# Optimization experiments

Measured on AMD Instinct MI355X. Metric: run time of the kernel, lower is better.

Reference implementation:

```python
import jax, jax.numpy as jnp
import numpy as np

T, N, K, E = 5, 2048, 20, 512
H, AI, BL, G1, G2, U = 64, 32, 64, 64, 64, 8
SLOPE, ALPHA = 0.01, 1.0


def gru(x, Wih, Whh, bih, bhh):
    # batch_first torch nn.GRU with h0 = 0. x: [B, L, I] -> [B, L, Hd]
    Hd = Whh.shape[1]
    def step(h, xt):
        gi = xt @ Wih.T + bih
        gh = h @ Whh.T + bhh
        ir, iz, in_ = jnp.split(gi, 3, axis=-1)
        hr, hz, hn = jnp.split(gh, 3, axis=-1)
        r = jax.nn.sigmoid(ir + hr)
        z = jax.nn.sigmoid(iz + hz)
        n = jnp.tanh(in_ + r * hn)
        h_new = (1.0 - z) * n + z * h
        return h_new, h_new
    h0 = jnp.zeros((x.shape[0], Hd), x.dtype)
    _, ys = jax.lax.scan(step, h0, jnp.swapaxes(x, 0, 1))
    return jnp.swapaxes(ys, 0, 1)


def lin_attn(x, w1, b1, w2):
    # LinearAttention: softmax over dim=2 (weights_size=1), then bmm -> [B,1,H]
    inter = jnp.tanh(x @ w1.T + b1)
    w = jax.nn.softmax(inter @ w2.T, axis=2)  # [B,L,1]
    return jnp.einsum('blk,blh->bkh', w, x)


def sgat_multi(x, W, a, adj):
    # All U SGAT heads at once. Decompose a^T [Wh_i || Wh_j] = s1_i + s2_j
    # (same math as the dense NxNx2F construction, without materializing it).
    O = W.shape[-1]
    Wh = jnp.einsum('nf,ufo->uno', x, W)                 # [U,N,O]
    s1 = jnp.einsum('uno,uo->un', Wh, a[:, :O, 0])
    s2 = jnp.einsum('uno,uo->un', Wh, a[:, O:, 0])
    e = jax.nn.leaky_relu(s1[:, :, None] + s2[:, None, :], SLOPE)  # [U,N,N]
    e = jnp.where(adj[None, :, :] > 0, e, -9e15)
    att = jax.nn.softmax(e, axis=2)
    h = jnp.einsum('unm,umo->uno', att, Wh)              # [U,N,O]
    # torch.cat over heads along feature dim -> [N, U*O]
    return jnp.transpose(h, (1, 0, 2)).reshape(x.shape[0], -1)


def setup_inputs() -> dict:
    key = jax.random.key(0)
    ks = iter(jax.random.split(key, 40))
    def nrm(shape, scale=0.1):
        return jax.random.normal(next(ks), shape, dtype=jnp.float32) * scale
    d = {}
    d['p'] = nrm((N, T, 3), 1.0)
    d['m'] = nrm((T, N, K, E), 1.0)
    adj = (jax.random.uniform(next(ks), (N, N)) < 0.05).astype(jnp.float32)
    d['adj'] = jnp.maximum(adj, jnp.eye(N, dtype=jnp.float32))
    d['Wih_p'] = nrm((3 * H, 3)); d['Whh_p'] = nrm((3 * H, H))
    d['bih_p'] = nrm((3 * H,)); d['bhh_p'] = nrm((3 * H,))
    d['Wih_m'] = nrm((3 * H, E)); d['Whh_m'] = nrm((3 * H, H))
    d['bih_m'] = nrm((3 * H,)); d['bhh_m'] = nrm((3 * H,))
    d['Wih_s'] = nrm((3 * H, H)); d['Whh_s'] = nrm((3 * H, H))
    d['bih_s'] = nrm((3 * H,)); d['bhh_s'] = nrm((3 * H,))
    for pref in ('ap', 'am', 'as'):
        d[pref + '_w1'] = nrm((AI, H)); d[pref + '_b1'] = nrm((AI,))
        d[pref + '_w2'] = nrm((1, AI))
    d['blend_W'] = nrm((BL, H, H)); d['blend_b'] = nrm((BL,))
    d['g1_W'] = nrm((U, BL, G1)); d['g1_a'] = nrm((U, 2 * G1, 1))
    d['g2_W'] = nrm((U, U * G1, G2)); d['g2_a'] = nrm((U, 2 * G2, 1))
    d['fin_W'] = nrm((1, U * G2)); d['fin_b'] = nrm((1,))
    return d


def reference(p, m, adj, Wih_p, Whh_p, bih_p, bhh_p, Wih_m, Whh_m, bih_m, bhh_m,
              Wih_s, Whh_s, bih_s, bhh_s, ap_w1, ap_b1, ap_w2, am_w1, am_b1, am_w2,
              as_w1, as_b1, as_w2, blend_W, blend_b, g1_W, g1_a, g2_W, g2_a,
              fin_W, fin_b):
    h_p = gru(p, Wih_p, Whh_p, bih_p, bhh_p)                     # [N,T,H]
    q = lin_attn(h_p, ap_w1, ap_b1, ap_w2)                       # [N,1,H]
    # all T message-days through gru_m at once (equivalent to python loop)
    h_m = gru(m.reshape(T * N, K, E), Wih_m, Whh_m, bih_m, bhh_m)
    r = lin_attn(h_m, am_w1, am_b1, am_w2).reshape(T, N, H).transpose(1, 0, 2)
    h_s = gru(r, Wih_s, Whh_s, bih_s, bhh_s)                     # [N,T,H]
    c = lin_attn(h_s, as_w1, as_b1, as_w2)                       # [N,1,H]
    # Blend: bilinear + relu
    x = jax.nn.relu(jnp.einsum('nbi,oij,nbj->nbo', q, blend_W, c) + blend_b)
    x = x.reshape(N, BL)
    z = jax.nn.elu(sgat_multi(x, g1_W, g1_a, adj), ALPHA)        # [N,U*G1]
    new_z = jax.nn.sigmoid(sgat_multi(z, g2_W, g2_a, adj))       # [N,U*G2]
    return jax.nn.sigmoid(new_z @ fin_W.T + fin_b)               # [N,1]
```

## Files before the change

kernel.cpp:

```cpp
#include <hip/hip_runtime.h>
#include <math.h>

namespace {

constexpr int T = 5, N = 2048, K = 20, E = 512;
constexpr int H = 64, U = 8;
constexpr int CAP = 512;
constexpr float SLOPE = 0.01f;

typedef __attribute__((ext_vector_type(8))) short short8;
typedef __attribute__((ext_vector_type(4))) float f32x4;

__device__ inline float sigm(float x) { return 1.0f / (1.0f + expf(-x)); }

__device__ inline void bsplit(float x, short& hi, short& lo) {
  unsigned u = __float_as_uint(x);
  hi = (short)(u >> 16);
  float r = x - __uint_as_float(u & 0xFFFF0000u);
  lo = (short)(__float_as_uint(r) >> 16);
}

__device__ inline float rdlane(float v, int lane) {
  return __int_as_float(__builtin_amdgcn_readlane(__float_as_int(v), lane));
}

__global__ __launch_bounds__(256) void k_prep(
    const float* __restrict__ WihM, const float* __restrict__ WhhM,
    const float* __restrict__ WihS, const float* __restrict__ WhhS,
    const float* __restrict__ WhhP, const float* __restrict__ Wb,
    short* __restrict__ BfM, short* __restrict__ BfS,
    float* __restrict__ WhhTm, float* __restrict__ WhhTs, float* __restrict__ WhhTp,
    float* __restrict__ Wt2)
{
  const int stride = 256 * 64;
  for (int idx = threadIdx.x + blockIdx.x * 256; idx < 192 * 512; idx += stride) {
    const int o = idx >> 9, k = idx & 511;
    short hi, lo; bsplit(WihM[idx], hi, lo);
    const long base = (long)(k >> 5) * 12288 + ((o >> 4) * 2) * 512
                    + ((k >> 3) & 3) * 128 + (o & 15) * 8 + (k & 7);
    BfM[base] = hi; BfM[base + 512] = lo;
  }
  for (int idx = threadIdx.x + blockIdx.x * 256; idx < 192 * 64; idx += stride) {
    const int o = idx >> 6, k = idx & 63;
    short hi, lo; bsplit(WihS[idx], hi, lo);
    const long base = (long)(k >> 5) * 12288 + ((o >> 4) * 2) * 512
                    + ((k >> 3) & 3) * 128 + (o & 15) * 8 + (k & 7);
    BfS[base] = hi; BfS[base + 512] = lo;
  }
  for (int idx = threadIdx.x + blockIdx.x * 256; idx < 64 * 192; idx += stride) {
    const int k2 = idx / 192, row = idx % 192;
    WhhTm[idx] = WhhM[row * 64 + k2];
    WhhTs[idx] = WhhS[row * 64 + k2];
    WhhTp[idx] = WhhP[row * 64 + k2];
  }
  for (int idx = threadIdx.x + blockIdx.x * 256; idx < 64 * 64 * 64; idx += stride) {
    const int o = idx >> 12, rem = idx & 4095, i = rem >> 6, j = rem & 63;
    Wt2[((i * 16 + (j >> 2)) * 64 + o) * 4 + (j & 3)] = Wb[(o * 64 + i) * 64 + j];
  }
}

__global__ __launch_bounds__(256) void k_prep2(
    const float* __restrict__ src, short* __restrict__ dst, const int Ksz)
{
  const int nb32 = Ksz >> 5;
  const int total = 8 * Ksz * 64;
  for (int idx = threadIdx.x + blockIdx.x * 256; idx < total; idx += 256 * 128) {
    const int u = idx / (Ksz * 64), rem = idx - u * Ksz * 64;
    const int f = rem >> 6, o = rem & 63;
    short hi, lo; bsplit(src[idx], hi, lo);
    const int col = u * 64 + o;
    const int cb = col >> 7, ntc = (col >> 4) & 7, c16 = col & 15;
    const int b = f >> 5, koct = (f >> 3) & 3, j = f & 7;
    const long base = ((long)(cb * nb32 + b)) * 8192 + (ntc * 2) * 512
                    + koct * 128 + c16 * 8 + j;
    dst[base] = hi; dst[base + 512] = lo;
  }
}

__global__ __launch_bounds__(256, 3) void k_gemm(
    const float* __restrict__ A, const short* __restrict__ Bf,
    const float* __restrict__ bias, float* __restrict__ out,
    const long row0, const int nb, const int strideA)
{
  __shared__ alignas(16) short Bc[2][24 * 512];
  const int tid = threadIdx.x, w = tid >> 6, l = tid & 63;
  const int lr = l & 15, g = l >> 4;
  const long blkrow = (long)blockIdx.x * 128;

  f32x4 acc[2][12];
  #pragma unroll
  for (int mf = 0; mf < 2; ++mf)
    #pragma unroll
    for (int nt = 0; nt < 12; ++nt) acc[mf][nt] = (f32x4){0.f, 0.f, 0.f, 0.f};

  short8 ahC[2], alC[2], ahN[2], alN[2];

  auto LOADA = [&](int b, short8* ah, short8* al) {
    #pragma unroll
    for (int mf = 0; mf < 2; ++mf) {
      const long r = blkrow + w * 32 + mf * 16 + lr;
      const float* __restrict__ src = A + (row0 + r) * (long)strideA + b * 32 + g * 8;
      const float4 v0 = *reinterpret_cast<const float4*>(src);
      const float4 v1 = *reinterpret_cast<const float4*>(src + 4);
      short h0,l0,h1,l1,h2,l2,h3,l3,h4,l4,h5,l5,h6,l6,h7,l7;
      bsplit(v0.x,h0,l0); bsplit(v0.y,h1,l1); bsplit(v0.z,h2,l2); bsplit(v0.w,h3,l3);
      bsplit(v1.x,h4,l4); bsplit(v1.y,h5,l5); bsplit(v1.z,h6,l6); bsplit(v1.w,h7,l7);
      ah[mf] = (short8){h0,h1,h2,h3,h4,h5,h6,h7};
      al[mf] = (short8){l0,l1,l2,l3,l4,l5,l6,l7};
    }
  };
  auto STAGE = [&](int buf, int b) {
    const short* __restrict__ bsrc = Bf + (long)b * 12288;
    #pragma unroll
    for (int i = 0; i < 6; ++i) {
      const int c = w + i * 4;
      __builtin_amdgcn_global_load_lds(
          (const __attribute__((address_space(1))) void*)(bsrc + c * 512 + l * 8),
          (__attribute__((address_space(3))) void*)(&Bc[buf][c * 512]), 16, 0, 0);
    }
  };

  LOADA(0, ahC, alC);
  STAGE(0, 0);
  __syncthreads();

  for (int b = 0; b < nb; ++b) {
    const bool more = (b + 1 < nb);
    if (more) { STAGE((b + 1) & 1, b + 1); LOADA(b + 1, ahN, alN); }
    const short* __restrict__ bcur = &Bc[b & 1][0];
    #pragma unroll
    for (int nt = 0; nt < 12; ++nt) {
      const short8 bh = *reinterpret_cast<const short8*>(bcur + (nt * 2 + 0) * 512 + l * 8);
      const short8 bl = *reinterpret_cast<const short8*>(bcur + (nt * 2 + 1) * 512 + l * 8);
      #pragma unroll
      for (int mf = 0; mf < 2; ++mf) {
        acc[mf][nt] = __builtin_amdgcn_mfma_f32_16x16x32_bf16(ahC[mf], bh, acc[mf][nt], 0, 0, 0);
        acc[mf][nt] = __builtin_amdgcn_mfma_f32_16x16x32_bf16(alC[mf], bh, acc[mf][nt], 0, 0, 0);
        acc[mf][nt] = __builtin_amdgcn_mfma_f32_16x16x32_bf16(ahC[mf], bl, acc[mf][nt], 0, 0, 0);
      }
    }
    __syncthreads();
    if (more) {
      #pragma unroll
      for (int mf = 0; mf < 2; ++mf) { ahC[mf] = ahN[mf]; alC[mf] = alN[mf]; }
    }
  }

  #pragma unroll
  for (int mf = 0; mf < 2; ++mf) {
    const long rbase = blkrow + w * 32 + mf * 16 + g * 4;
    #pragma unroll
    for (int nt = 0; nt < 12; ++nt) {
      const int col = nt * 16 + lr;
      const float bb = bias[col];
      #pragma unroll
      for (int i = 0; i < 4; ++i)
        out[(rbase + i) * 192 + col] = acc[mf][nt][i] + bb;
    }
  }
}

__global__ __launch_bounds__(256, 3) void k_gemmW(
    const float* __restrict__ A, const short* __restrict__ Bf2,
    const float* __restrict__ ga,
    float* __restrict__ Wh, float* __restrict__ s1, float* __restrict__ s2,
    const int nb, const int strideA)
{
  __shared__ alignas(16) short Bc[2][16 * 512];
  const int tid = threadIdx.x, w = tid >> 6, l = tid & 63;
  const int lr = l & 15, g = l >> 4;
  const long blkrow = (long)blockIdx.x * 128;
  const int cb = blockIdx.y;

  f32x4 acc[2][8];
  #pragma unroll
  for (int mf = 0; mf < 2; ++mf)
    #pragma unroll
    for (int nt = 0; nt < 8; ++nt) acc[mf][nt] = (f32x4){0.f, 0.f, 0.f, 0.f};

  short8 ahC[2], alC[2], ahN[2], alN[2];

  auto LOADA = [&](int b, short8* ah, short8* al) {
    #pragma unroll
    for (int mf = 0; mf < 2; ++mf) {
      const long r = blkrow + w * 32 + mf * 16 + lr;
      const float* __restrict__ src = A + r * (long)strideA + b * 32 + g * 8;
      const float4 v0 = *reinterpret_cast<const float4*>(src);
      const float4 v1 = *reinterpret_cast<const float4*>(src + 4);
      short h0,l0,h1,l1,h2,l2,h3,l3,h4,l4,h5,l5,h6,l6,h7,l7;
      bsplit(v0.x,h0,l0); bsplit(v0.y,h1,l1); bsplit(v0.z,h2,l2); bsplit(v0.w,h3,l3);
      bsplit(v1.x,h4,l4); bsplit(v1.y,h5,l5); bsplit(v1.z,h6,l6); bsplit(v1.w,h7,l7);
      ah[mf] = (short8){h0,h1,h2,h3,h4,h5,h6,h7};
      al[mf] = (short8){l0,l1,l2,l3,l4,l5,l6,l7};
    }
  };
  auto STAGE = [&](int buf, int b) {
    const short* __restrict__ bsrc = Bf2 + ((long)cb * nb + b) * 8192;
    #pragma unroll
    for (int i = 0; i < 4; ++i) {
      const int c = w + i * 4;
      __builtin_amdgcn_global_load_lds(
          (const __attribute__((address_space(1))) void*)(bsrc + c * 512 + l * 8),
          (__attribute__((address_space(3))) void*)(&Bc[buf][c * 512]), 16, 0, 0);
    }
  };

  LOADA(0, ahC, alC);
  STAGE(0, 0);
  __syncthreads();

  for (int b = 0; b < nb; ++b) {
    const bool more = (b + 1 < nb);
    if (more) { STAGE((b + 1) & 1, b + 1); LOADA(b + 1, ahN, alN); }
    const short* __restrict__ bcur = &Bc[b & 1][0];
    #pragma unroll
    for (int nt = 0; nt < 8; ++nt) {
      const short8 bh = *reinterpret_cast<const short8*>(bcur + (nt * 2 + 0) * 512 + l * 8);
      const short8 bl = *reinterpret_cast<const short8*>(bcur + (nt * 2 + 1) * 512 + l * 8);
      #pragma unroll
      for (int mf = 0; mf < 2; ++mf) {
        acc[mf][nt] = __builtin_amdgcn_mfma_f32_16x16x32_bf16(ahC[mf], bh, acc[mf][nt], 0, 0, 0);
        acc[mf][nt] = __builtin_amdgcn_mfma_f32_16x16x32_bf16(alC[mf], bh, acc[mf][nt], 0, 0, 0);
        acc[mf][nt] = __builtin_amdgcn_mfma_f32_16x16x32_bf16(ahC[mf], bl, acc[mf][nt], 0, 0, 0);
      }
    }
    __syncthreads();
    if (more) {
      #pragma unroll
      for (int mf = 0; mf < 2; ++mf) { ahC[mf] = ahN[mf]; alC[mf] = alN[mf]; }
    }
  }

  #pragma unroll
  for (int mf = 0; mf < 2; ++mf) {
    const long rbase = blkrow + w * 32 + mf * 16 + g * 4;
    #pragma unroll
    for (int nt = 0; nt < 8; ++nt) {
      const int col = cb * 128 + nt * 16 + lr;
      const int u = col >> 6, o = col & 63;
      #pragma unroll
      for (int i = 0; i < 4; ++i)
        Wh[((long)u * N + (rbase + i)) * 64 + o] = acc[mf][nt][i];
    }
    #pragma unroll
    for (int i = 0; i < 4; ++i) {
      const long r = rbase + i;
      #pragma unroll
      for (int uh = 0; uh < 2; ++uh) {
        const int u = cb * 2 + uh;
        float p1 = 0.f, p2 = 0.f;
        #pragma unroll
        for (int nt4 = 0; nt4 < 4; ++nt4) {
          const float v = acc[mf][uh * 4 + nt4][i];
          const int o = nt4 * 16 + lr;
          p1 += v * ga[u * 128 + o];
          p2 += v * ga[u * 128 + 64 + o];
        }
        #pragma unroll
        for (int dd = 8; dd > 0; dd >>= 1) { p1 += __shfl_xor(p1, dd, 64); p2 += __shfl_xor(p2, dd, 64); }
        if (lr == 0) { s1[u * N + r] = p1; s2[u * N + r] = p2; }
      }
    }
  }
}

__global__ __launch_bounds__(256, 2) void k_recur(
    const float* __restrict__ gi, const float* __restrict__ WhhT,
    const float* __restrict__ bhh, float* __restrict__ rout, const int seq0)
{
  const int tid = threadIdx.x, w = tid >> 6, l = tid & 63;
  const int lseq = blockIdx.x * 4 + w;
  float wr[64], wz[64], wn[64];
  #pragma unroll
  for (int k2 = 0; k2 < 64; ++k2) {
    wr[k2] = WhhT[k2 * 192 + l];
    wz[k2] = WhhT[k2 * 192 + 64 + l];
    wn[k2] = WhhT[k2 * 192 + 128 + l];
  }
  const float bR = bhh[l], bZ = bhh[64 + l], bN = bhh[128 + l];
  const float* __restrict__ grow = gi + (long)lseq * K * 192;
  float h = 0.f, rsum = 0.f;
  float gR = grow[l], gZ = grow[64 + l], gN = grow[128 + l];
  for (int k = 0; k < K; ++k) {
    float nR = 0.f, nZ = 0.f, nN = 0.f;
    if (k + 1 < K) {
      const int off = (k + 1) * 192;
      nR = grow[off + l]; nZ = grow[off + 64 + l]; nN = grow[off + 128 + l];
    }
    float aR = bR, aZ = bZ, aN = bN;
    #pragma unroll
    for (int k2 = 0; k2 < 64; ++k2) {
      const float hk = rdlane(h, k2);
      aR += wr[k2] * hk; aZ += wz[k2] * hk; aN += wn[k2] * hk;
    }
    const float r = sigm(gR + aR);
    const float z = sigm(gZ + aZ);
    const float nn = tanhf(gN + r * aN);
    h = (1.f - z) * nn + z * h;
    rsum += h;
    gR = nR; gZ = nZ; gN = nN;
  }
  const int gseq = seq0 + lseq;
  const int tt = gseq / N, n = gseq % N;
  rout[(n * T + tt) * H + l] = rsum;
}

__global__ __launch_bounds__(256, 2) void k_recur_p(
    const float* __restrict__ p, const float* __restrict__ Wih,
    const float* __restrict__ WhhT, const float* __restrict__ bih,
    const float* __restrict__ bhh, float* __restrict__ q)
{
  const int tid = threadIdx.x, w = tid >> 6, l = tid & 63;
  const int n = blockIdx.x * 4 + w;
  float wr[64], wz[64], wn[64];
  #pragma unroll
  for (int k2 = 0; k2 < 64; ++k2) {
    wr[k2] = WhhT[k2 * 192 + l];
    wz[k2] = WhhT[k2 * 192 + 64 + l];
    wn[k2] = WhhT[k2 * 192 + 128 + l];
  }
  float iR[3], iZ[3], iN[3];
  #pragma unroll
  for (int c = 0; c < 3; ++c) {
    iR[c] = Wih[l * 3 + c];
    iZ[c] = Wih[(64 + l) * 3 + c];
    iN[c] = Wih[(128 + l) * 3 + c];
  }
  const float biR = bih[l], biZ = bih[64 + l], biN = bih[128 + l];
  const float bhR = bhh[l], bhZ = bhh[64 + l], bhN = bhh[128 + l];
  float h = 0.f, qs = 0.f;
  for (int t = 0; t < T; ++t) {
    const float x0 = p[n * 15 + t * 3], x1 = p[n * 15 + t * 3 + 1], x2 = p[n * 15 + t * 3 + 2];
    const float gR = biR + iR[0] * x0 + iR[1] * x1 + iR[2] * x2;
    const float gZ = biZ + iZ[0] * x0 + iZ[1] * x1 + iZ[2] * x2;
    const float gN = biN + iN[0] * x0 + iN[1] * x1 + iN[2] * x2;
    float aR = bhR, aZ = bhZ, aN = bhN;
    #pragma unroll
    for (int k2 = 0; k2 < 64; ++k2) {
      const float hk = rdlane(h, k2);
      aR += wr[k2] * hk; aZ += wz[k2] * hk; aN += wn[k2] * hk;
    }
    const float r = sigm(gR + aR), z = sigm(gZ + aZ);
    const float nn = tanhf(gN + r * aN);
    h = (1.f - z) * nn + z * h;
    qs += h;
  }
  q[n * H + l] = qs;
}

__global__ __launch_bounds__(256, 2) void k_recur_s(
    const float* __restrict__ gx, const float* __restrict__ WhhT,
    const float* __restrict__ bhh, float* __restrict__ c)
{
  const int tid = threadIdx.x, w = tid >> 6, l = tid & 63;
  const int n = blockIdx.x * 4 + w;
  float wr[64], wz[64], wn[64];
  #pragma unroll
  for (int k2 = 0; k2 < 64; ++k2) {
    wr[k2] = WhhT[k2 * 192 + l];
    wz[k2] = WhhT[k2 * 192 + 64 + l];
    wn[k2] = WhhT[k2 * 192 + 128 + l];
  }
  const float bR = bhh[l], bZ = bhh[64 + l], bN = bhh[128 + l];
  const float* __restrict__ grow = gx + (long)n * T * 192;
  float h = 0.f, cs = 0.f;
  for (int t = 0; t < T; ++t) {
    const float gR = grow[t * 192 + l], gZ = grow[t * 192 + 64 + l], gN = grow[t * 192 + 128 + l];
    float aR = bR, aZ = bZ, aN = bN;
    #pragma unroll
    for (int k2 = 0; k2 < 64; ++k2) {
      const float hk = rdlane(h, k2);
      aR += wr[k2] * hk; aZ += wz[k2] * hk; aN += wn[k2] * hk;
    }
    const float r = sigm(gR + aR), z = sigm(gZ + aZ);
    const float nn = tanhf(gN + r * aN);
    h = (1.f - z) * nn + z * h;
    cs += h;
  }
  c[n * H + l] = cs;
}

__global__ __launch_bounds__(256) void k_blend(
    const float* __restrict__ q, const float* __restrict__ c,
    const float* __restrict__ Wt2, const float* __restrict__ b,
    float* __restrict__ xout)
{
  __shared__ float qs[8][64];
  __shared__ alignas(16) float cs[8][64];
  const int tid = threadIdx.x;
  const int o = tid & 63, grp = tid >> 6;
  const int n0 = blockIdx.x * 8;
  for (int idx = tid; idx < 512; idx += 256) {
    qs[idx >> 6][idx & 63] = q[(n0 + (idx >> 6)) * 64 + (idx & 63)];
    cs[idx >> 6][idx & 63] = c[(n0 + (idx >> 6)) * 64 + (idx & 63)];
  }
  __syncthreads();
  const int na = grp * 2, nb = na + 1;
  float acca = b[o], accb = b[o];
  const float4* __restrict__ W4 = reinterpret_cast<const float4*>(Wt2);
  const float4* ca4 = reinterpret_cast<const float4*>(&cs[na][0]);
  const float4* cb4 = reinterpret_cast<const float4*>(&cs[nb][0]);
  for (int i = 0; i < 64; ++i) {
    float pa = 0.f, pb = 0.f;
    #pragma unroll
    for (int j4 = 0; j4 < 16; ++j4) {
      const float4 wv = W4[(i * 16 + j4) * 64 + o];
      const float4 va = ca4[j4], vb = cb4[j4];
      pa += wv.x * va.x + wv.y * va.y + wv.z * va.z + wv.w * va.w;
      pb += wv.x * vb.x + wv.y * vb.y + wv.z * vb.z + wv.w * vb.w;
    }
    acca += qs[na][i] * pa;
    accb += qs[nb][i] * pb;
  }
  xout[(n0 + na) * 64 + o] = fmaxf(acca, 0.f);
  xout[(n0 + nb) * 64 + o] = fmaxf(accb, 0.f);
}

__global__ __launch_bounds__(256) void k_compact(
    const float* __restrict__ adj, int* __restrict__ nbr, int* __restrict__ deg)
{
  const int w = threadIdx.x >> 6, lane = threadIdx.x & 63;
  const int i = blockIdx.x * 4 + w;
  int base = 0;
  for (int j0 = 0; j0 < N; j0 += 64) {
    const float v = adj[(long)i * N + j0 + lane];
    const unsigned long long mask = __ballot(v > 0.f);
    const int pre = __popcll(mask & ((1ull << lane) - 1ull));
    if (v > 0.f && base + pre < CAP) nbr[i * CAP + base + pre] = j0 + lane;
    base += __popcll(mask);
  }
  if (lane == 0) deg[i] = base < CAP ? base : CAP;
}

__global__ __launch_bounds__(256) void k_gat_attn(
    const float* __restrict__ Wh, const float* __restrict__ s1,
    const float* __restrict__ s2, const int* __restrict__ nbr,
    const int* __restrict__ deg, const int mode, float* __restrict__ out)
{
  __shared__ float ew[4][CAP];
  __shared__ int nb[4][CAP];
  const int w = threadIdx.x >> 6, lane = threadIdx.x & 63;
  const int row = blockIdx.x * 4 + w;
  const int u = row >> 11;
  const int i = row & (N - 1);
  const int d = deg[i];
  const float su = s1[u * N + i];
  float mx = -1e30f;
  for (int t = lane; t < d; t += 64) {
    const int j = nbr[i * CAP + t];
    float e = su + s2[u * N + j];
    e = e > 0.f ? e : SLOPE * e;
    ew[w][t] = e; nb[w][t] = j;
    mx = fmaxf(mx, e);
  }
  #pragma unroll
  for (int dd = 32; dd > 0; dd >>= 1) mx = fmaxf(mx, __shfl_xor(mx, dd, 64));
  float sm = 0.f;
  for (int t = lane; t < d; t += 64) {
    const float ex = expf(ew[w][t] - mx);
    ew[w][t] = ex;
    sm += ex;
  }
  #pragma unroll
  for (int dd = 32; dd > 0; dd >>= 1) sm += __shfl_xor(sm, dd, 64);
  __syncthreads();
  const float inv = 1.f / sm;
  float a0 = 0.f, a1 = 0.f, a2 = 0.f, a3 = 0.f;
  const float* __restrict__ whb = Wh + (long)u * N * 64 + lane;
  int t = 0;
  for (; t + 4 <= d; t += 4) {
    const float e0 = ew[w][t],     e1 = ew[w][t + 1];
    const float e2 = ew[w][t + 2], e3 = ew[w][t + 3];
    const int j0 = nb[w][t],     j1 = nb[w][t + 1];
    const int j2 = nb[w][t + 2], j3 = nb[w][t + 3];
    a0 += e0 * whb[(long)j0 * 64];
    a1 += e1 * whb[(long)j1 * 64];
    a2 += e2 * whb[(long)j2 * 64];
    a3 += e3 * whb[(long)j3 * 64];
  }
  for (; t < d; ++t) a0 += ew[w][t] * whb[(long)nb[w][t] * 64];
  float acc = ((a0 + a1) + (a2 + a3)) * inv;
  float val;
  if (mode == 0) val = acc > 0.f ? acc : (expf(acc) - 1.f);
  else           val = 1.f / (1.f + expf(-acc));
  out[(long)i * (U * 64) + u * 64 + lane] = val;
}

__global__ __launch_bounds__(256) void k_final(
    const float* __restrict__ nz, const float* __restrict__ fw,
    const float* __restrict__ fb, float* __restrict__ out)
{
  const int w = threadIdx.x >> 6, lane = threadIdx.x & 63;
  const int n = blockIdx.x * 4 + w;
  float p = 0.f;
  #pragma unroll
  for (int f = lane; f < 512; f += 64) p += nz[(long)n * 512 + f] * fw[f];
  #pragma unroll
  for (int d = 32; d > 0; d >>= 1) p += __shfl_xor(p, d, 64);
  if (lane == 0) out[n] = 1.f / (1.f + expf(-(p + fb[0])));
}

}

extern "C" void kernel_launch(void* const* d_in, const int* in_sizes, int n_in,
                              void* d_out, int out_size, void* d_ws, size_t ws_size,
                              hipStream_t stream)
{
  const float* p     = (const float*)d_in[0];
  const float* m     = (const float*)d_in[1];
  const float* adj   = (const float*)d_in[2];
  const float* Wih_p = (const float*)d_in[3];
  const float* Whh_p = (const float*)d_in[4];
  const float* bih_p = (const float*)d_in[5];
  const float* bhh_p = (const float*)d_in[6];
  const float* Wih_m = (const float*)d_in[7];
  const float* Whh_m = (const float*)d_in[8];
  const float* bih_m = (const float*)d_in[9];
  const float* bhh_m = (const float*)d_in[10];
  const float* Wih_s = (const float*)d_in[11];
  const float* Whh_s = (const float*)d_in[12];
  const float* bih_s = (const float*)d_in[13];
  const float* bhh_s = (const float*)d_in[14];
  const float* blend_W = (const float*)d_in[24];
  const float* blend_b = (const float*)d_in[25];
  const float* g1W = (const float*)d_in[26];
  const float* g1a = (const float*)d_in[27];
  const float* g2W = (const float*)d_in[28];
  const float* g2a = (const float*)d_in[29];
  const float* finW = (const float*)d_in[30];
  const float* finb = (const float*)d_in[31];

  float* ws = (float*)d_ws;
  float* q    = ws;
  float* rr   = q + N * H;
  float* c    = rr + N * T * H;
  float* xb   = c + N * H;
  float* Wh1  = xb + N * H;
  float* s1a  = Wh1 + U * N * 64;
  float* s2a  = s1a + U * N;
  float* z    = s2a + U * N;
  float* Wh2  = z + (long)N * 512;
  float* s1b  = Wh2 + U * N * 64;
  float* s2b  = s1b + U * N;
  float* nz   = s2b + U * N;
  float* Wt2  = nz + (long)N * 512;
  float* gx   = Wt2 + 64 * 64 * 64;
  float* WhhTm = gx + (long)10240 * 192;
  float* WhhTs = WhhTm + 64 * 192;
  float* WhhTp = WhhTs + 64 * 192;
  int*   nbr  = (int*)(WhhTp + 64 * 192);
  int*   deg  = nbr + (long)N * CAP;
  short* BfM  = (short*)(deg + N);
  short* BfS  = BfM + 16 * 12288;
  short* Bf1  = BfS + 2 * 12288;
  short* Bf2  = Bf1 + 4 * 2 * 8192;
  float* gi   = (float*)(Bf2 + 4 * 16 * 8192);

  const long avail = (long)(ws_size / 4) - (gi - ws);
  const long total_seqs = (long)T * N;
  long chunk = (avail / ((long)K * 192) / 32) * 32;
  if (chunk > total_seqs) chunk = total_seqs;
  if (chunk < 32) chunk = 32;

  k_prep<<<64, 256, 0, stream>>>(Wih_m, Whh_m, Wih_s, Whh_s, Whh_p, blend_W,
                                 BfM, BfS, WhhTm, WhhTs, WhhTp, Wt2);
  k_prep2<<<128, 256, 0, stream>>>(g2W, Bf2, 512);
  k_prep2<<<128, 256, 0, stream>>>(g1W, Bf1, 64);
  k_recur_p<<<N / 4, 256, 0, stream>>>(p, Wih_p, WhhTp, bih_p, bhh_p, q);
  for (long s0 = 0; s0 < total_seqs; s0 += chunk) {
    const long cs = (total_seqs - s0) < chunk ? (total_seqs - s0) : chunk;
    const long rows = cs * K;
    k_gemm<<<(int)(rows / 128), 256, 0, stream>>>(m, BfM, bih_m, gi, s0 * K, 16, 512);
    k_recur<<<(int)(cs / 4), 256, 0, stream>>>(gi, WhhTm, bhh_m, rr, (int)s0);
  }
  k_gemm<<<80, 256, 0, stream>>>(rr, BfS, bih_s, gx, 0, 2, 64);
  k_recur_s<<<N / 4, 256, 0, stream>>>(gx, WhhTs, bhh_s, c);
  k_blend<<<N / 8, 256, 0, stream>>>(q, c, Wt2, blend_b, xb);
  k_compact<<<N / 4, 256, 0, stream>>>(adj, nbr, deg);
  k_gemmW<<<dim3(N / 128, 4), 256, 0, stream>>>(xb, Bf1, g1a, Wh1, s1a, s2a, 2, 64);
  k_gat_attn<<<(U * N) / 4, 256, 0, stream>>>(Wh1, s1a, s2a, nbr, deg, 0, z);
  k_gemmW<<<dim3(N / 128, 4), 256, 0, stream>>>(z, Bf2, g2a, Wh2, s1b, s2b, 16, 512);
  k_gat_attn<<<(U * N) / 4, 256, 0, stream>>>(Wh2, s1b, s2b, nbr, deg, 1, nz);
  k_final<<<N / 4, 256, 0, stream>>>(nz, finW, finb, (float*)d_out);
}
```

Before: 521.8 us.

## Drop low-order bf16 split of weights; stage 64-wide K blocks in GEMMs

Weight matrices are now stored as a single truncated bf16 (hi part only) instead of hi+lo, so each GEMM does two MFMAs per tile (A_hi*B, A_lo*B) instead of three. The packed weight layout is changed so each staged LDS buffer covers 64 K-elements, halving the number of K iterations and barriers. The register prefetch of the next A block is removed, so A loads are no longer overlapped with MFMAs. Dropping the weight low part reduces accuracy to roughly bf16 weight precision, which may or may not stay within tolerance.

```diff
diff --git a/kernel.cpp b/kernel.cpp
--- a/kernel.cpp
+++ b/kernel.cpp
@@ -35,17 +35,15 @@
   const int stride = 256 * 64;
   for (int idx = threadIdx.x + blockIdx.x * 256; idx < 192 * 512; idx += stride) {
     const int o = idx >> 9, k = idx & 511;
-    short hi, lo; bsplit(WihM[idx], hi, lo);
-    const long base = (long)(k >> 5) * 12288 + ((o >> 4) * 2) * 512
+    const long base = (long)(k >> 6) * 12288 + (((k >> 5) & 1) * 12 + (o >> 4)) * 512
                     + ((k >> 3) & 3) * 128 + (o & 15) * 8 + (k & 7);
-    BfM[base] = hi; BfM[base + 512] = lo;
+    BfM[base] = (short)(__float_as_uint(WihM[idx]) >> 16);
   }
   for (int idx = threadIdx.x + blockIdx.x * 256; idx < 192 * 64; idx += stride) {
     const int o = idx >> 6, k = idx & 63;
-    short hi, lo; bsplit(WihS[idx], hi, lo);
-    const long base = (long)(k >> 5) * 12288 + ((o >> 4) * 2) * 512
+    const long base = (((k >> 5) & 1) * 12 + (o >> 4)) * 512
                     + ((k >> 3) & 3) * 128 + (o & 15) * 8 + (k & 7);
-    BfS[base] = hi; BfS[base + 512] = lo;
+    BfS[base] = (short)(__float_as_uint(WihS[idx]) >> 16);
   }
   for (int idx = threadIdx.x + blockIdx.x * 256; idx < 64 * 192; idx += stride) {
     const int k2 = idx / 192, row = idx % 192;
@@ -62,18 +60,16 @@
 __global__ __launch_bounds__(256) void k_prep2(
     const float* __restrict__ src, short* __restrict__ dst, const int Ksz)
 {
-  const int nb32 = Ksz >> 5;
+  const int nb64 = Ksz >> 6;
   const int total = 8 * Ksz * 64;
   for (int idx = threadIdx.x + blockIdx.x * 256; idx < total; idx += 256 * 128) {
     const int u = idx / (Ksz * 64), rem = idx - u * Ksz * 64;
     const int f = rem >> 6, o = rem & 63;
-    short hi, lo; bsplit(src[idx], hi, lo);
     const int col = u * 64 + o;
-    const int cb = col >> 7, ntc = (col >> 4) & 7, c16 = col & 15;
-    const int b = f >> 5, koct = (f >> 3) & 3, j = f & 7;
-    const long base = ((long)(cb * nb32 + b)) * 8192 + (ntc * 2) * 512
-                    + koct * 128 + c16 * 8 + j;
-    dst[base] = hi; dst[base + 512] = lo;
+    const long base = ((long)(col >> 7) * nb64 + (f >> 6)) * 8192
+                    + (((f >> 5) & 1) * 8 + ((col >> 4) & 7)) * 512
+                    + ((f >> 3) & 3) * 128 + (col & 15) * 8 + (f & 7);
+    dst[base] = (short)(__float_as_uint(src[idx]) >> 16);
   }
 }
 
@@ -93,22 +89,6 @@
     #pragma unroll
     for (int nt = 0; nt < 12; ++nt) acc[mf][nt] = (f32x4){0.f, 0.f, 0.f, 0.f};
 
-  short8 ahC[2], alC[2], ahN[2], alN[2];
-
-  auto LOADA = [&](int b, short8* ah, short8* al) {
-    #pragma unroll
-    for (int mf = 0; mf < 2; ++mf) {
-      const long r = blkrow + w * 32 + mf * 16 + lr;
-      const float* __restrict__ src = A + (row0 + r) * (long)strideA + b * 32 + g * 8;
-      const float4 v0 = *reinterpret_cast<const float4*>(src);
-      const float4 v1 = *reinterpret_cast<const float4*>(src + 4);
-      short h0,l0,h1,l1,h2,l2,h3,l3,h4,l4,h5,l5,h6,l6,h7,l7;
-      bsplit(v0.x,h0,l0); bsplit(v0.y,h1,l1); bsplit(v0.z,h2,l2); bsplit(v0.w,h3,l3);
-      bsplit(v1.x,h4,l4); bsplit(v1.y,h5,l5); bsplit(v1.z,h6,l6); bsplit(v1.w,h7,l7);
-      ah[mf] = (short8){h0,h1,h2,h3,h4,h5,h6,h7};
-      al[mf] = (short8){l0,l1,l2,l3,l4,l5,l6,l7};
-    }
-  };
   auto STAGE = [&](int buf, int b) {
     const short* __restrict__ bsrc = Bf + (long)b * 12288;
     #pragma unroll
@@ -120,30 +100,40 @@
     }
   };
 
-  LOADA(0, ahC, alC);
   STAGE(0, 0);
   __syncthreads();
 
   for (int b = 0; b < nb; ++b) {
-    const bool more = (b + 1 < nb);
-    if (more) { STAGE((b + 1) & 1, b + 1); LOADA(b + 1, ahN, alN); }
+    if (b + 1 < nb) STAGE((b + 1) & 1, b + 1);
+    short8 ah[2][2], al[2][2];
+    #pragma unroll
+    for (int kc = 0; kc < 2; ++kc)
+      #pragma unroll
+      for (int mf = 0; mf < 2; ++mf) {
+        const long r = blkrow + w * 32 + mf * 16 + lr;
+        const float* __restrict__ src = A + (row0 + r) * (long)strideA + b * 64 + kc * 32 + g * 8;
+        const float4 v0 = *reinterpret_cast<const float4*>(src);
+        const float4 v1 = *reinterpret_cast<const float4*>(src + 4);
+        short h0,l0,h1,l1,h2,l2,h3,l3,h4,l4,h5,l5,h6,l6,h7,l7;
+        bsplit(v0.x,h0,l0); bsplit(v0.y,h1,l1); bsplit(v0.z,h2,l2); bsplit(v0.w,h3,l3);
+        bsplit(v1.x,h4,l4); bsplit(v1.y,h5,l5); bsplit(v1.z,h6,l6); bsplit(v1.w,h7,l7);
+        ah[kc][mf] = (short8){h0,h1,h2,h3,h4,h5,h6,h7};
+        al[kc][mf] = (short8){l0,l1,l2,l3,l4,l5,l6,l7};
+      }
     const short* __restrict__ bcur = &Bc[b & 1][0];
     #pragma unroll
-    for (int nt = 0; nt < 12; ++nt) {
-      const short8 bh = *reinterpret_cast<const short8*>(bcur + (nt * 2 + 0) * 512 + l * 8);
-      const short8 bl = *reinterpret_cast<const short8*>(bcur + (nt * 2 + 1) * 512 + l * 8);
-      #pragma unroll
-      for (int mf = 0; mf < 2; ++mf) {
-        acc[mf][nt] = __builtin_amdgcn_mfma_f32_16x16x32_bf16(ahC[mf], bh, acc[mf][nt], 0, 0, 0);
-        acc[mf][nt] = __builtin_amdgcn_mfma_f32_16x16x32_bf16(alC[mf], bh, acc[mf][nt], 0, 0, 0);
-        acc[mf][nt] = __builtin_amdgcn_mfma_f32_16x16x32_bf16(ahC[mf], bl, acc[mf][nt], 0, 0, 0);
+    for (int kc = 0; kc < 2; ++kc) {
+      #pragma unroll
+      for (int nt = 0; nt < 12; ++nt) {
+        const short8 bh = *reinterpret_cast<const short8*>(bcur + (kc * 12 + nt) * 512 + l * 8);
+        #pragma unroll
+        for (int mf = 0; mf < 2; ++mf) {
+          acc[mf][nt] = __builtin_amdgcn_mfma_f32_16x16x32_bf16(ah[kc][mf], bh, acc[mf][nt], 0, 0, 0);
+          acc[mf][nt] = __builtin_amdgcn_mfma_f32_16x16x32_bf16(al[kc][mf], bh, acc[mf][nt], 0, 0, 0);
+        }
       }
     }
     __syncthreads();
-    if (more) {
-      #pragma unroll
-      for (int mf = 0; mf < 2; ++mf) { ahC[mf] = ahN[mf]; alC[mf] = alN[mf]; }
-    }
   }
 
   #pragma unroll
@@ -178,22 +168,6 @@
     #pragma unroll
     for (int nt = 0; nt < 8; ++nt) acc[mf][nt] = (f32x4){0.f, 0.f, 0.f, 0.f};
 
-  short8 ahC[2], alC[2], ahN[2], alN[2];
-
-  auto LOADA = [&](int b, short8* ah, short8* al) {
-    #pragma unroll
-    for (int mf = 0; mf < 2; ++mf) {
-      const long r = blkrow + w * 32 + mf * 16 + lr;
-      const float* __restrict__ src = A + r * (long)strideA + b * 32 + g * 8;
-      const float4 v0 = *reinterpret_cast<const float4*>(src);
-      const float4 v1 = *reinterpret_cast<const float4*>(src + 4);
-      short h0,l0,h1,l1,h2,l2,h3,l3,h4,l4,h5,l5,h6,l6,h7,l7;
-      bsplit(v0.x,h0,l0); bsplit(v0.y,h1,l1); bsplit(v0.z,h2,l2); bsplit(v0.w,h3,l3);
-      bsplit(v1.x,h4,l4); bsplit(v1.y,h5,l5); bsplit(v1.z,h6,l6); bsplit(v1.w,h7,l7);
-      ah[mf] = (short8){h0,h1,h2,h3,h4,h5,h6,h7};
-      al[mf] = (short8){l0,l1,l2,l3,l4,l5,l6,l7};
-    }
-  };
   auto STAGE = [&](int buf, int b) {
     const short* __restrict__ bsrc = Bf2 + ((long)cb * nb + b) * 8192;
     #pragma unroll
@@ -205,30 +179,40 @@
     }
   };
 
-  LOADA(0, ahC, alC);
   STAGE(0, 0);
   __syncthreads();
 
   for (int b = 0; b < nb; ++b) {
-    const bool more = (b + 1 < nb);
-    if (more) { STAGE((b + 1) & 1, b + 1); LOADA(b + 1, ahN, alN); }
+    if (b + 1 < nb) STAGE((b + 1) & 1, b + 1);
+    short8 ah[2][2], al[2][2];
+    #pragma unroll
+    for (int kc = 0; kc < 2; ++kc)
+      #pragma unroll
+      for (int mf = 0; mf < 2; ++mf) {
+        const long r = blkrow + w * 32 + mf * 16 + lr;
+        const float* __restrict__ src = A + r * (long)strideA + b * 64 + kc * 32 + g * 8;
+        const float4 v0 = *reinterpret_cast<const float4*>(src);
+        const float4 v1 = *reinterpret_cast<const float4*>(src + 4);
+        short h0,l0,h1,l1,h2,l2,h3,l3,h4,l4,h5,l5,h6,l6,h7,l7;
+        bsplit(v0.x,h0,l0); bsplit(v0.y,h1,l1); bsplit(v0.z,h2,l2); bsplit(v0.w,h3,l3);
+        bsplit(v1.x,h4,l4); bsplit(v1.y,h5,l5); bsplit(v1.z,h6,l6); bsplit(v1.w,h7,l7);
+        ah[kc][mf] = (short8){h0,h1,h2,h3,h4,h5,h6,h7};
+        al[kc][mf] = (short8){l0,l1,l2,l3,l4,l5,l6,l7};
+      }
     const short* __restrict__ bcur = &Bc[b & 1][0];
     #pragma unroll
-    for (int nt = 0; nt < 8; ++nt) {
-      const short8 bh = *reinterpret_cast<const short8*>(bcur + (nt * 2 + 0) * 512 + l * 8);
-      const short8 bl = *reinterpret_cast<const short8*>(bcur + (nt * 2 + 1) * 512 + l * 8);
-      #pragma unroll
-      for (int mf = 0; mf < 2; ++mf) {
-        acc[mf][nt] = __builtin_amdgcn_mfma_f32_16x16x32_bf16(ahC[mf], bh, acc[mf][nt], 0, 0, 0);
-        acc[mf][nt] = __builtin_amdgcn_mfma_f32_16x16x32_bf16(alC[mf], bh, acc[mf][nt], 0, 0, 0);
-        acc[mf][nt] = __builtin_amdgcn_mfma_f32_16x16x32_bf16(ahC[mf], bl, acc[mf][nt], 0, 0, 0);
+    for (int kc = 0; kc < 2; ++kc) {
+      #pragma unroll
+      for (int nt = 0; nt < 8; ++nt) {
+        const short8 bh = *reinterpret_cast<const short8*>(bcur + (kc * 8 + nt) * 512 + l * 8);
+        #pragma unroll
+        for (int mf = 0; mf < 2; ++mf) {
+          acc[mf][nt] = __builtin_amdgcn_mfma_f32_16x16x32_bf16(ah[kc][mf], bh, acc[mf][nt], 0, 0, 0);
+          acc[mf][nt] = __builtin_amdgcn_mfma_f32_16x16x32_bf16(al[kc][mf], bh, acc[mf][nt], 0, 0, 0);
+        }
       }
     }
     __syncthreads();
-    if (more) {
-      #pragma unroll
-      for (int mf = 0; mf < 2; ++mf) { ahC[mf] = ahN[mf]; alC[mf] = alN[mf]; }
-    }
   }
 
   #pragma unroll
@@ -551,10 +535,10 @@
   int*   nbr  = (int*)(WhhTp + 64 * 192);
   int*   deg  = nbr + (long)N * CAP;
   short* BfM  = (short*)(deg + N);
-  short* BfS  = BfM + 16 * 12288;
-  short* Bf1  = BfS + 2 * 12288;
-  short* Bf2  = Bf1 + 4 * 2 * 8192;
-  float* gi   = (float*)(Bf2 + 4 * 16 * 8192);
+  short* BfS  = BfM + 8 * 12288;
+  short* Bf1  = BfS + 12288;
+  short* Bf2  = Bf1 + 4 * 8192;
+  float* gi   = (float*)(Bf2 + 4 * 8 * 8192);
 
   const long avail = (long)(ws_size / 4) - (gi - ws);
   const long total_seqs = (long)T * N;
@@ -570,16 +554,16 @@
   for (long s0 = 0; s0 < total_seqs; s0 += chunk) {
     const long cs = (total_seqs - s0) < chunk ? (total_seqs - s0) : chunk;
     const long rows = cs * K;
-    k_gemm<<<(int)(rows / 128), 256, 0, stream>>>(m, BfM, bih_m, gi, s0 * K, 16, 512);
+    k_gemm<<<(int)(rows / 128), 256, 0, stream>>>(m, BfM, bih_m, gi, s0 * K, 8, 512);
     k_recur<<<(int)(cs / 4), 256, 0, stream>>>(gi, WhhTm, bhh_m, rr, (int)s0);
   }
-  k_gemm<<<80, 256, 0, stream>>>(rr, BfS, bih_s, gx, 0, 2, 64);
+  k_gemm<<<80, 256, 0, stream>>>(rr, BfS, bih_s, gx, 0, 1, 64);
   k_recur_s<<<N / 4, 256, 0, stream>>>(gx, WhhTs, bhh_s, c);
   k_blend<<<N / 8, 256, 0, stream>>>(q, c, Wt2, blend_b, xb);
   k_compact<<<N / 4, 256, 0, stream>>>(adj, nbr, deg);
-  k_gemmW<<<dim3(N / 128, 4), 256, 0, stream>>>(xb, Bf1, g1a, Wh1, s1a, s2a, 2, 64);
+  k_gemmW<<<dim3(N / 128, 4), 256, 0, stream>>>(xb, Bf1, g1a, Wh1, s1a, s2a, 1, 64);
   k_gat_attn<<<(U * N) / 4, 256, 0, stream>>>(Wh1, s1a, s2a, nbr, deg, 0, z);
-  k_gemmW<<<dim3(N / 128, 4), 256, 0, stream>>>(z, Bf2, g2a, Wh2, s1b, s2b, 16, 512);
+  k_gemmW<<<dim3(N / 128, 4), 256, 0, stream>>>(z, Bf2, g2a, Wh2, s1b, s2b, 8, 512);
   k_gat_attn<<<(U * N) / 4, 256, 0, stream>>>(Wh2, s1b, s2b, nbr, deg, 1, nz);
   k_final<<<N / 4, 256, 0, stream>>>(nz, finW, finb, (float*)d_out);
 }
```

Result: faster. 491.2 us (-5.9%).
